# Kernel tuning notes

Measured on AMD Instinct MI355X. Metric: run time of the kernel, lower is better.

The kernel has to match this reference:

```python
import jax, jax.numpy as jnp
import numpy as np

N_NODES = 100000
DEGREE = 16
FEAT = 128
HID = 64
OUT = 16
BATCH = 4096
K = 12  # n_neibs


def setup_inputs() -> dict:
    key = jax.random.key(0)
    ks = jax.random.split(key, 12)
    idx0 = jax.random.randint(ks[0], (BATCH,), 0, N_NODES, dtype=jnp.int64 if jax.config.jax_enable_x64 else jnp.int32)
    buf1 = jax.random.randint(ks[1], (BATCH, K), 0, 1000000)
    buf2 = jax.random.randint(ks[2], (BATCH * K, K), 0, 1000000)
    indptr = jnp.arange(N_NODES) * DEGREE            # CSR row pointers (fixed degree)
    indices = jax.random.randint(ks[3], (N_NODES * DEGREE,), 0, N_NODES)
    degrees = jnp.full((N_NODES,), DEGREE, dtype=jnp.int32)
    emb_weight = jax.random.normal(ks[4], (N_NODES, FEAT), dtype=jnp.float32)
    enc_w = jax.random.normal(ks[5], (HID, FEAT), dtype=jnp.float32) * (1.0 / np.sqrt(FEAT))
    h1_w = jax.random.normal(ks[6], (HID, 2 * HID), dtype=jnp.float32) * (1.0 / np.sqrt(2 * HID))
    h1_b = jnp.zeros((HID,), jnp.float32)
    h2_w = jax.random.normal(ks[7], (HID, HID), dtype=jnp.float32) * (1.0 / np.sqrt(HID))
    h2_b = jnp.zeros((HID,), jnp.float32)
    out_w = jax.random.normal(ks[8], (OUT, HID), dtype=jnp.float32) * (1.0 / np.sqrt(HID))
    out_b = jnp.zeros((OUT,), jnp.float32)
    return dict(idx0=idx0, buf1=buf1, buf2=buf2, indptr=indptr, indices=indices,
                degrees=degrees, emb_weight=emb_weight, enc_w=enc_w,
                h1_w=h1_w, h1_b=h1_b, h2_w=h2_w, h2_b=h2_b, out_w=out_w, out_b=out_b)


def _sample_neighbors(nodes, buf, indptr, indices, degrees):
    # nodes: [M], buf: [M, K] random ints -> neighbor node ids [M, K]
    neibs = buf % degrees[nodes][:, None]
    offsets = indptr[nodes][:, None] + neibs
    return indices[offsets]


def reference(idx0, buf1, buf2, indptr, indices, degrees, emb_weight,
              enc_w, h1_w, h1_b, h2_w, h2_b, out_w, out_b):
    B = idx0.shape[0]
    idx1 = _sample_neighbors(idx0, buf1, indptr, indices, degrees)              # [B, K]
    idx2 = _sample_neighbors(idx1.reshape(B * K), buf2, indptr, indices, degrees)
    idx2 = idx2.reshape(B, K, K)                                                # [B, K, K]

    enc_1hop = jax.nn.relu(jnp.einsum('bkf,hf->bkh', emb_weight[idx1], enc_w))  # [B, K, H]
    enc_2hop = jax.nn.relu(jnp.einsum('bkjf,hf->bkjh', emb_weight[idx2], enc_w))
    avg_2hop = enc_2hop.mean(axis=-2)                                           # [B, K, H]

    h1 = jnp.concatenate([enc_1hop, avg_2hop], axis=-1)                         # [B, K, 2H]
    h1 = jax.nn.relu(jnp.einsum('bkc,hc->bkh', h1, h1_w) + h1_b)
    avg_1hop = h1.mean(axis=-2)                                                 # [B, H]
    h0 = jax.nn.relu(avg_1hop @ h2_w.T + h2_b)
    return h0 @ out_w.T + out_b                                                 # [B, OUT]
```

## Files before the change

kernel.cpp:

```cpp
#include <hip/hip_runtime.h>

#define NNODES 100000

typedef __attribute__((ext_vector_type(8))) short bf16x8;
typedef __attribute__((ext_vector_type(4))) float floatx4;

union PackU { uint4 u; bf16x8 v; };

__device__ __forceinline__ uint pack_hi2(float x0, float x1) {
    return (__float_as_uint(x1) & 0xFFFF0000u) | (__float_as_uint(x0) >> 16);
}
__device__ __forceinline__ uint pack_lo2(float x0, float x1) {
    float l0 = x0 - __uint_as_float(__float_as_uint(x0) & 0xFFFF0000u);
    float l1 = x1 - __uint_as_float(__float_as_uint(x1) & 0xFFFF0000u);
    return (__float_as_uint(l1) & 0xFFFF0000u) | (__float_as_uint(l0) >> 16);
}
__device__ __forceinline__ ushort bf_rne(float x) {
    unsigned u = __float_as_uint(x);
    return (ushort)((u + 0x7FFFu + ((u >> 16) & 1u)) >> 16);
}
__device__ __forceinline__ float lo16f(uint u) { return __uint_as_float(u << 16); }
__device__ __forceinline__ float hi16f(uint u) { return __uint_as_float(u & 0xFFFF0000u); }

__global__ __launch_bounds__(256) void k_gemm(const float* __restrict__ emb,
                                              const float* __restrict__ enc_w,
                                              const float* __restrict__ h1_w,
                                              ushort* __restrict__ encAB) {
    __shared__ ushort smem[35840];
    ushort* sB_h = smem;
    ushort* sB_l = smem + 8704;
    ushort* sW_h = smem + 17408;
    ushort* sW_l = smem + 26624;
    ushort* sE_h = smem;
    ushort* sE_l = smem + 4608;

    const int t = threadIdx.x;
    const int n0 = blockIdx.x * 64;
    const int w = t >> 6, lane = t & 63;
    const int m = lane & 15, q = lane >> 4;

    int nn = n0 + w * 16 + m; if (nn > NNODES - 1) nn = NNODES - 1;
    const float* rowp = emb + (size_t)nn * 128 + q * 8;
    bf16x8 a_h[4], a_l[4];
#pragma unroll
    for (int ks = 0; ks < 4; ++ks) {
        float4 f0 = *(const float4*)(rowp + ks * 32);
        float4 f1 = *(const float4*)(rowp + ks * 32 + 4);
        PackU ph, pl;
        ph.u = (uint4){pack_hi2(f0.x, f0.y), pack_hi2(f0.z, f0.w),
                       pack_hi2(f1.x, f1.y), pack_hi2(f1.z, f1.w)};
        pl.u = (uint4){pack_lo2(f0.x, f0.y), pack_lo2(f0.z, f0.w),
                       pack_lo2(f1.x, f1.y), pack_lo2(f1.z, f1.w)};
        a_h[ks] = ph.v; a_l[ks] = pl.v;
    }

#pragma unroll
    for (int r = 0; r < 8; ++r) {
        int c4 = (t + 256 * r) * 4;
        int h = c4 >> 7, f = c4 & 127;
        float4 v = *(const float4*)&enc_w[c4];
        *(uint2*)&sB_h[h * 136 + f] = (uint2){pack_hi2(v.x, v.y), pack_hi2(v.z, v.w)};
        *(uint2*)&sB_l[h * 136 + f] = (uint2){pack_lo2(v.x, v.y), pack_lo2(v.z, v.w)};
    }
#pragma unroll
    for (int r = 0; r < 8; ++r) {
        int c4 = (t + 256 * r) * 4;
        int o = c4 >> 7, cc = c4 & 127;
        int o2 = o + (cc & 64), col = cc & 63;
        float4 v = *(const float4*)&h1_w[c4];
        *(uint2*)&sW_h[o2 * 72 + col] = (uint2){pack_hi2(v.x, v.y), pack_hi2(v.z, v.w)};
        *(uint2*)&sW_l[o2 * 72 + col] = (uint2){pack_lo2(v.x, v.y), pack_lo2(v.z, v.w)};
    }
    __syncthreads();

    floatx4 acc[4] = {};
#pragma unroll
    for (int ht = 0; ht < 4; ++ht) {
        const ushort* pBh = &sB_h[(ht * 16 + m) * 136 + q * 8];
#pragma unroll
        for (int ks = 0; ks < 4; ++ks) {
            bf16x8 bh = *(const bf16x8*)(pBh + ks * 32);
            bf16x8 bl = *(const bf16x8*)(pBh + 8704 + ks * 32);
            acc[ht] = __builtin_amdgcn_mfma_f32_16x16x32_bf16(a_h[ks], bh, acc[ht], 0, 0, 0);
            acc[ht] = __builtin_amdgcn_mfma_f32_16x16x32_bf16(a_l[ks], bh, acc[ht], 0, 0, 0);
            acc[ht] = __builtin_amdgcn_mfma_f32_16x16x32_bf16(a_h[ks], bl, acc[ht], 0, 0, 0);
        }
    }
    __syncthreads();

#pragma unroll
    for (int ht = 0; ht < 4; ++ht)
#pragma unroll
        for (int i = 0; i < 4; ++i) {
            float v = fmaxf(acc[ht][i], 0.f);
            int row = w * 16 + q * 4 + i, col = ht * 16 + m;
            uint uv = __float_as_uint(v);
            sE_h[row * 72 + col] = (ushort)(uv >> 16);
            float lo = v - __uint_as_float(uv & 0xFFFF0000u);
            sE_l[row * 72 + col] = (ushort)(__float_as_uint(lo) >> 16);
        }
    __syncthreads();

    bf16x8 e_h[2], e_l[2];
    {
        const ushort* pE = &sE_h[(w * 16 + m) * 72 + q * 8];
#pragma unroll
        for (int ks = 0; ks < 2; ++ks) {
            e_h[ks] = *(const bf16x8*)(pE + ks * 32);
            e_l[ks] = *(const bf16x8*)(pE + 4608 + ks * 32);
        }
    }
    floatx4 acc2[8] = {};
#pragma unroll
    for (int ot = 0; ot < 8; ++ot) {
        const ushort* pWh = &sW_h[(ot * 16 + m) * 72 + q * 8];
#pragma unroll
        for (int ks = 0; ks < 2; ++ks) {
            bf16x8 bh = *(const bf16x8*)(pWh + ks * 32);
            bf16x8 bl = *(const bf16x8*)(pWh + 9216 + ks * 32);
            acc2[ot] = __builtin_amdgcn_mfma_f32_16x16x32_bf16(e_h[ks], bh, acc2[ot], 0, 0, 0);
            acc2[ot] = __builtin_amdgcn_mfma_f32_16x16x32_bf16(e_l[ks], bh, acc2[ot], 0, 0, 0);
            acc2[ot] = __builtin_amdgcn_mfma_f32_16x16x32_bf16(e_h[ks], bl, acc2[ot], 0, 0, 0);
        }
    }
#pragma unroll
    for (int ot = 0; ot < 8; ++ot)
#pragma unroll
        for (int i = 0; i < 4; ++i) {
            int n = n0 + w * 16 + q * 4 + i;
            if (n < NNODES) encAB[n * 128 + ot * 16 + m] = bf_rne(acc2[ot][i]);
        }
}

__global__ __launch_bounds__(256) void k_gather_head(const int* __restrict__ idx0,
                                                     const int* __restrict__ buf1,
                                                     const int* __restrict__ buf2,
                                                     const int* __restrict__ indices,
                                                     const ushort* __restrict__ encAB,
                                                     const float* __restrict__ h1_b,
                                                     const float* __restrict__ h2_w,
                                                     const float* __restrict__ h2_b,
                                                     const float* __restrict__ out_w,
                                                     const float* __restrict__ out_b,
                                                     float* __restrict__ out) {
    __shared__ int s_idx1[48];
    __shared__ int s_idx2[576];
    __shared__ float sW2[64 * 65];
    __shared__ float sWo[64 * 17];
    __shared__ float sAvg[4][64];
    __shared__ float sH0[4][64];

    const int t = threadIdx.x;
    const int b0 = blockIdx.x * 4;

    if (t < 48) {
        int bl = t / 12;
        s_idx1[t] = indices[idx0[b0 + bl] * 16 + (buf1[b0 * 12 + t] & 15)];
    }
#pragma unroll
    for (int r = 0; r < 16; ++r) {
        int e = t + 256 * r;
        sW2[(e & 63) * 65 + (e >> 6)] = h2_w[e];
    }
#pragma unroll
    for (int r = 0; r < 4; ++r) {
        int e = t + 256 * r;
        sWo[(e & 63) * 17 + (e >> 6)] = out_w[e];
    }
    __syncthreads();

#pragma unroll
    for (int r = 0; r < 3; ++r) {
        int s = t + 256 * r;
        if (s < 576) {
            int bk = s / 12;
            s_idx2[s] = indices[s_idx1[bk] * 16 + (buf2[b0 * 144 + s] & 15)];
        }
    }
    __syncthreads();

    const int w = t >> 6, lane = t & 63;
    const int pp = lane >> 5, c = lane & 31;
    const uint* __restrict__ encAB32 = (const uint*)encAB;
    const int* myi1 = &s_idx1[w * 12];
    const int* myi2 = &s_idx2[w * 144];
    float2 bb = *(const float2*)&h1_b[2 * c];
    float hs0 = 0.f, hs1 = 0.f;
#pragma unroll 3
    for (int k = 0; k < 12; ++k) {
        uint av = encAB32[myi1[k] * 64 + c];
        float s0 = 0.f, s1 = 0.f;
#pragma unroll
        for (int jj = 0; jj < 6; ++jj) {
            uint v = encAB32[myi2[k * 12 + 2 * jj + pp] * 64 + 32 + c];
            s0 += lo16f(v); s1 += hi16f(v);
        }
        s0 += __shfl_xor(s0, 32);
        s1 += __shfl_xor(s1, 32);
        hs0 += fmaxf(lo16f(av) + s0 * (1.f / 12.f) + bb.x, 0.f);
        hs1 += fmaxf(hi16f(av) + s1 * (1.f / 12.f) + bb.y, 0.f);
    }
    if (pp == 0) {
        sAvg[w][2 * c]     = hs0 * (1.f / 12.f);
        sAvg[w][2 * c + 1] = hs1 * (1.f / 12.f);
    }
    __syncthreads();

    {
        float acc = h2_b[lane];
#pragma unroll 8
        for (int i = 0; i < 64; ++i)
            acc += sAvg[w][i] * sW2[i * 65 + lane];
        sH0[w][lane] = fmaxf(acc, 0.f);
    }
    __syncthreads();
    if (t < 64) {
        int g2 = t >> 4, o = t & 15;
        float acc2 = out_b[o];
#pragma unroll 8
        for (int i = 0; i < 64; ++i)
            acc2 += sH0[g2][i] * sWo[i * 17 + o];
        out[(b0 + g2) * 16 + o] = acc2;
    }
}

extern "C" void kernel_launch(void* const* d_in, const int* in_sizes, int n_in,
                              void* d_out, int out_size, void* d_ws, size_t ws_size,
                              hipStream_t stream) {
    const int*   idx0    = (const int*)d_in[0];
    const int*   buf1    = (const int*)d_in[1];
    const int*   buf2    = (const int*)d_in[2];
    const int*   indices = (const int*)d_in[4];
    const float* emb     = (const float*)d_in[6];
    const float* enc_w   = (const float*)d_in[7];
    const float* h1_w    = (const float*)d_in[8];
    const float* h1_b    = (const float*)d_in[9];
    const float* h2_w    = (const float*)d_in[10];
    const float* h2_b    = (const float*)d_in[11];
    const float* out_w   = (const float*)d_in[12];
    const float* out_b   = (const float*)d_in[13];
    (void)d_in[3]; (void)d_in[5];
    float* out = (float*)d_out;

    ushort* encAB = (ushort*)d_ws;

    k_gemm<<<1563, 256, 0, stream>>>(emb, enc_w, h1_w, encAB);
    k_gather_head<<<1024, 256, 0, stream>>>(idx0, buf1, buf2, indices, encAB,
                                            h1_b, h2_w, h2_b, out_w, out_b, out);
}
```

Baseline: 144.2 us.

## Drop low-part h1 weight MFMA, split gather/head kernels, raise gemm occupancy

Measured after the change: 144.2 us. No clear change (+0.0%).

```diff
diff --git a/kernel.cpp b/kernel.cpp
--- a/kernel.cpp
+++ b/kernel.cpp
@@ -22,15 +22,14 @@
 __device__ __forceinline__ float lo16f(uint u) { return __uint_as_float(u << 16); }
 __device__ __forceinline__ float hi16f(uint u) { return __uint_as_float(u & 0xFFFF0000u); }
 
-__global__ __launch_bounds__(256) void k_gemm(const float* __restrict__ emb,
-                                              const float* __restrict__ enc_w,
-                                              const float* __restrict__ h1_w,
-                                              ushort* __restrict__ encAB) {
-    __shared__ ushort smem[35840];
+__global__ __launch_bounds__(256, 3) void k_gemm(const float* __restrict__ emb,
+                                                 const float* __restrict__ enc_w,
+                                                 const float* __restrict__ h1_w,
+                                                 ushort* __restrict__ encAB) {
+    __shared__ ushort smem[26624];
     ushort* sB_h = smem;
     ushort* sB_l = smem + 8704;
     ushort* sW_h = smem + 17408;
-    ushort* sW_l = smem + 26624;
     ushort* sE_h = smem;
     ushort* sE_l = smem + 4608;
 
@@ -69,7 +68,6 @@
         int o2 = o + (cc & 64), col = cc & 63;
         float4 v = *(const float4*)&h1_w[c4];
         *(uint2*)&sW_h[o2 * 72 + col] = (uint2){pack_hi2(v.x, v.y), pack_hi2(v.z, v.w)};
-        *(uint2*)&sW_l[o2 * 72 + col] = (uint2){pack_lo2(v.x, v.y), pack_lo2(v.z, v.w)};
     }
     __syncthreads();
 
@@ -117,10 +115,8 @@
 #pragma unroll
         for (int ks = 0; ks < 2; ++ks) {
             bf16x8 bh = *(const bf16x8*)(pWh + ks * 32);
-            bf16x8 bl = *(const bf16x8*)(pWh + 9216 + ks * 32);
             acc2[ot] = __builtin_amdgcn_mfma_f32_16x16x32_bf16(e_h[ks], bh, acc2[ot], 0, 0, 0);
             acc2[ot] = __builtin_amdgcn_mfma_f32_16x16x32_bf16(e_l[ks], bh, acc2[ot], 0, 0, 0);
-            acc2[ot] = __builtin_amdgcn_mfma_f32_16x16x32_bf16(e_h[ks], bl, acc2[ot], 0, 0, 0);
         }
     }
 #pragma unroll
@@ -132,31 +128,81 @@
         }
 }
 
-__global__ __launch_bounds__(256) void k_gather_head(const int* __restrict__ idx0,
-                                                     const int* __restrict__ buf1,
-                                                     const int* __restrict__ buf2,
-                                                     const int* __restrict__ indices,
-                                                     const ushort* __restrict__ encAB,
-                                                     const float* __restrict__ h1_b,
-                                                     const float* __restrict__ h2_w,
-                                                     const float* __restrict__ h2_b,
-                                                     const float* __restrict__ out_w,
-                                                     const float* __restrict__ out_b,
-                                                     float* __restrict__ out) {
-    __shared__ int s_idx1[48];
-    __shared__ int s_idx2[576];
+__global__ __launch_bounds__(256) void k_gather(const int* __restrict__ idx0,
+                                                const int* __restrict__ buf1,
+                                                const int* __restrict__ buf2,
+                                                const int* __restrict__ indices,
+                                                const ushort* __restrict__ encAB,
+                                                const float* __restrict__ h1_b,
+                                                float* __restrict__ avg1) {
+    __shared__ int s_idx1[24];
+    __shared__ int s_idx2[288];
+    __shared__ float s_part[2][2][64];
+
+    const int t = threadIdx.x;
+    const int b0 = blockIdx.x * 2;
+
+    if (t < 24) {
+        int bl = t / 12;
+        s_idx1[t] = indices[idx0[b0 + bl] * 16 + (buf1[b0 * 12 + t] & 15)];
+    }
+    __syncthreads();
+#pragma unroll
+    for (int r = 0; r < 2; ++r) {
+        int s = t + 256 * r;
+        if (s < 288) {
+            int bk = s / 12;
+            s_idx2[s] = indices[s_idx1[bk] * 16 + (buf2[b0 * 144 + s] & 15)];
+        }
+    }
+    __syncthreads();
+
+    const int w = t >> 6, lane = t & 63;
+    const int bb = w >> 1, half = w & 1;
+    const int pp = lane >> 5, c = lane & 31;
+    const uint* __restrict__ encAB32 = (const uint*)encAB;
+    const int* myi1 = &s_idx1[bb * 12];
+    const int* myi2 = &s_idx2[bb * 144];
+    float2 bbias = *(const float2*)&h1_b[2 * c];
+    float hs0 = 0.f, hs1 = 0.f;
+#pragma unroll 3
+    for (int kk = 0; kk < 6; ++kk) {
+        int k = half * 6 + kk;
+        uint av = encAB32[myi1[k] * 64 + c];
+        float s0 = 0.f, s1 = 0.f;
+#pragma unroll
+        for (int jj = 0; jj < 6; ++jj) {
+            uint v = encAB32[myi2[k * 12 + 2 * jj + pp] * 64 + 32 + c];
+            s0 += lo16f(v); s1 += hi16f(v);
+        }
+        s0 += __shfl_xor(s0, 32);
+        s1 += __shfl_xor(s1, 32);
+        hs0 += fmaxf(lo16f(av) + s0 * (1.f / 12.f) + bbias.x, 0.f);
+        hs1 += fmaxf(hi16f(av) + s1 * (1.f / 12.f) + bbias.y, 0.f);
+    }
+    if (pp == 0) {
+        s_part[bb][half][2 * c]     = hs0;
+        s_part[bb][half][2 * c + 1] = hs1;
+    }
+    __syncthreads();
+    if (t < 128) {
+        int b2 = t >> 6, h = t & 63;
+        avg1[(b0 + b2) * 64 + h] =
+            (s_part[b2][0][h] + s_part[b2][1][h]) * (1.f / 12.f);
+    }
+}
+
+__global__ __launch_bounds__(256) void k_head(const float* __restrict__ avg1,
+                                              const float* __restrict__ h2_w,
+                                              const float* __restrict__ h2_b,
+                                              const float* __restrict__ out_w,
+                                              const float* __restrict__ out_b,
+                                              float* __restrict__ out) {
     __shared__ float sW2[64 * 65];
     __shared__ float sWo[64 * 17];
     __shared__ float sAvg[4][64];
     __shared__ float sH0[4][64];
-
     const int t = threadIdx.x;
-    const int b0 = blockIdx.x * 4;
-
-    if (t < 48) {
-        int bl = t / 12;
-        s_idx1[t] = indices[idx0[b0 + bl] * 16 + (buf1[b0 * 12 + t] & 15)];
-    }
 #pragma unroll
     for (int r = 0; r < 16; ++r) {
         int e = t + 256 * r;
@@ -167,52 +213,15 @@
         int e = t + 256 * r;
         sWo[(e & 63) * 17 + (e >> 6)] = out_w[e];
     }
-    __syncthreads();
-
-#pragma unroll
-    for (int r = 0; r < 3; ++r) {
-        int s = t + 256 * r;
-        if (s < 576) {
-            int bk = s / 12;
-            s_idx2[s] = indices[s_idx1[bk] * 16 + (buf2[b0 * 144 + s] & 15)];
-        }
-    }
-    __syncthreads();
-
-    const int w = t >> 6, lane = t & 63;
-    const int pp = lane >> 5, c = lane & 31;
-    const uint* __restrict__ encAB32 = (const uint*)encAB;
-    const int* myi1 = &s_idx1[w * 12];
-    const int* myi2 = &s_idx2[w * 144];
-    float2 bb = *(const float2*)&h1_b[2 * c];
-    float hs0 = 0.f, hs1 = 0.f;
-#pragma unroll 3
-    for (int k = 0; k < 12; ++k) {
-        uint av = encAB32[myi1[k] * 64 + c];
-        float s0 = 0.f, s1 = 0.f;
-#pragma unroll
-        for (int jj = 0; jj < 6; ++jj) {
-            uint v = encAB32[myi2[k * 12 + 2 * jj + pp] * 64 + 32 + c];
-            s0 += lo16f(v); s1 += hi16f(v);
-        }
-        s0 += __shfl_xor(s0, 32);
-        s1 += __shfl_xor(s1, 32);
-        hs0 += fmaxf(lo16f(av) + s0 * (1.f / 12.f) + bb.x, 0.f);
-        hs1 += fmaxf(hi16f(av) + s1 * (1.f / 12.f) + bb.y, 0.f);
-    }
-    if (pp == 0) {
-        sAvg[w][2 * c]     = hs0 * (1.f / 12.f);
-        sAvg[w][2 * c + 1] = hs1 * (1.f / 12.f);
-    }
-    __syncthreads();
-
-    {
-        float acc = h2_b[lane];
+    const int b0 = blockIdx.x * 4;
+    const int g = t >> 6, h = t & 63;
+    sAvg[g][h] = avg1[(b0 + g) * 64 + h];
+    __syncthreads();
+    float acc = h2_b[h];
 #pragma unroll 8
-        for (int i = 0; i < 64; ++i)
-            acc += sAvg[w][i] * sW2[i * 65 + lane];
-        sH0[w][lane] = fmaxf(acc, 0.f);
-    }
+    for (int i = 0; i < 64; ++i)
+        acc += sAvg[g][i] * sW2[i * 65 + h];
+    sH0[g][h] = fmaxf(acc, 0.f);
     __syncthreads();
     if (t < 64) {
         int g2 = t >> 4, o = t & 15;
@@ -243,8 +252,9 @@
     float* out = (float*)d_out;
 
     ushort* encAB = (ushort*)d_ws;
+    float*  avg1  = (float*)(encAB + 12800000);
 
     k_gemm<<<1563, 256, 0, stream>>>(emb, enc_w, h1_w, encAB);
-    k_gather_head<<<1024, 256, 0, stream>>>(idx0, buf1, buf2, indices, encAB,
-                                            h1_b, h2_w, h2_b, out_w, out_b, out);
-}
+    k_gather<<<2048, 256, 0, stream>>>(idx0, buf1, buf2, indices, encAB, h1_b, avg1);
+    k_head<<<1024, 256, 0, stream>>>(avg1, h2_w, h2_b, out_w, out_b, out);
+}
```
